# Kernel tuning notes

Measured on AMD Instinct MI355X. Metric: run time of the kernel, lower is better.

The kernel has to match this reference:

```python
import jax, jax.numpy as jnp
import numpy as np

N, E, G = 50000, 800000, 64
IN_CH, HID = 64, 64


def setup_inputs() -> dict:
    key = jax.random.key(0)
    ks = jax.random.split(key, 16)
    inp = {
        "x": jax.random.normal(ks[0], (N, IN_CH), dtype=jnp.float32),
        "edge_index": jax.random.randint(ks[1], (2, E), 0, N, dtype=jnp.int64),
        "edge_weight": jax.random.uniform(ks[2], (E,), dtype=jnp.float32),
        "batch": jnp.sort(jax.random.randint(ks[3], (N,), 0, G, dtype=jnp.int64)),
        "W1": jax.random.normal(ks[4], (IN_CH, HID), dtype=jnp.float32) / np.sqrt(IN_CH),
        "b1": jnp.zeros((HID,), dtype=jnp.float32),
        "W2": jax.random.normal(ks[5], (HID, HID), dtype=jnp.float32) / np.sqrt(HID),
        "b2": jnp.zeros((HID,), dtype=jnp.float32),
        "W3": jax.random.normal(ks[6], (HID, HID), dtype=jnp.float32) / np.sqrt(HID),
        "b3": jnp.zeros((HID,), dtype=jnp.float32),
        "lw1": jax.random.normal(ks[7], (HID, HID // 2), dtype=jnp.float32) / np.sqrt(HID),
        "lb1": jnp.zeros((HID // 2,), dtype=jnp.float32),
        "lw2": jax.random.normal(ks[8], (HID // 2, HID // 4), dtype=jnp.float32) / np.sqrt(HID // 2),
        "lb2": jnp.zeros((HID // 4,), dtype=jnp.float32),
        "lw3": jax.random.normal(ks[9], (HID // 4, 1), dtype=jnp.float32) / np.sqrt(HID // 4),
        "lb3": jnp.zeros((1,), dtype=jnp.float32),
    }
    return inp


def _gcn_layer(x, W, b, src, dst, ew):
    # GCNConv with normalize=False: transform, gather at src, weight, scatter-add at dst, + bias
    h = x @ W                                  # [N, HID]
    msg = h[src] * ew[:, None]                 # [E, HID] gather + edge weighting
    agg = jax.ops.segment_sum(msg, dst, num_segments=N)  # [N, HID] scatter-add
    return agg + b


def reference(x, edge_index, edge_weight, batch,
              W1, b1, W2, b2, W3, b3,
              lw1, lb1, lw2, lb2, lw3, lb3):
    src, dst = edge_index[0], edge_index[1]
    h = jax.nn.relu(_gcn_layer(x, W1, b1, src, dst, edge_weight))
    h = jax.nn.relu(_gcn_layer(h, W2, b2, src, dst, edge_weight))
    h = jax.nn.relu(_gcn_layer(h, W3, b3, src, dst, edge_weight))
    # global mean pool over graphs
    sums = jax.ops.segment_sum(h, batch, num_segments=G)          # [G, HID]
    cnts = jax.ops.segment_sum(jnp.ones((N,), h.dtype), batch, num_segments=G)
    pooled = sums / jnp.clip(cnts, 1.0)[:, None]
    # MLP head (dropout is identity in eval mode)
    z = jax.nn.relu(pooled @ lw1 + lb1)
    z = jax.nn.relu(z @ lw2 + lb2)
    return z @ lw3 + lb3                       # [G, 1]
```

## Files before the change

kernel.cpp:

```cpp
#include <hip/hip_runtime.h>
#include <hip/hip_bf16.h>
#include <hip/hip_fp16.h>


#define HID 64
#define KNBLK 256

__global__ __launch_bounds__(256) void histA_conv_kernel(const int* __restrict__ ei,
                                                         int* __restrict__ counts,
                                                         const float* __restrict__ x,
                                                         __half* __restrict__ xh,
                                                         int E, int K, int chunk, int n4) {
    __shared__ int hist[256];
    int t = threadIdx.x, b = blockIdx.x;
    hist[t] = 0;
    __syncthreads();
    int s = b * chunk, e1 = min(E, s + chunk);
    for (int i = s + t; i < e1; i += 256)
        atomicAdd(&hist[ei[E + i] >> 8], 1);
    for (int i = b * 256 + t; i < n4; i += 256 * KNBLK) {
        const float4 v = *reinterpret_cast<const float4*>(x + (size_t)i * 4);
        __half2 a = __float22half2_rn(make_float2(v.x, v.y));
        __half2 b2 = __float22half2_rn(make_float2(v.z, v.w));
        uint2 u;
        u.x = __builtin_bit_cast(unsigned int, a);
        u.y = __builtin_bit_cast(unsigned int, b2);
        *reinterpret_cast<uint2*>(xh + (size_t)i * 4) = u;
    }
    __syncthreads();
    if (t < K) counts[b * K + t] = hist[t];
}

__global__ __launch_bounds__(256) void scanB1_kernel(int* __restrict__ counts,
                                                     int* __restrict__ btot, int K) {
    __shared__ int sh[256];
    int k = blockIdx.x, t = threadIdx.x;
    int v = counts[t * K + k];
    sh[t] = v;
    __syncthreads();
    #pragma unroll
    for (int d = 1; d < 256; d <<= 1) {
        int add = (t >= d) ? sh[t - d] : 0;
        __syncthreads();
        sh[t] += add;
        __syncthreads();
    }
    counts[t * K + k] = sh[t] - v;
    if (t == 255) btot[k] = sh[255];
}

__global__ __launch_bounds__(256) void scanB2_kernel(const int* __restrict__ btot,
                                                     int* __restrict__ bb0, int K,
                                                     float* __restrict__ sums,
                                                     float* __restrict__ cnts, int G) {
    __shared__ int sh[256];
    int t = threadIdx.x;
    int v = (t < K) ? btot[t] : 0;
    sh[t] = v;
    __syncthreads();
    #pragma unroll
    for (int d = 1; d < 256; d <<= 1) {
        int add = (t >= d) ? sh[t - d] : 0;
        __syncthreads();
        sh[t] += add;
        __syncthreads();
    }
    if (t < K) bb0[t] = sh[t] - v;
    if (t == 255) bb0[K] = sh[255];
    for (int i = t; i < G * 64; i += 256) sums[i] = 0.f;
    if (t < G) cnts[t] = 0.f;
}

__global__ __launch_bounds__(256) void passB_kernel(const int* __restrict__ ei,
                                                    const float* __restrict__ ew,
                                                    const int* __restrict__ counts,
                                                    const int* __restrict__ bb0,
                                                    int2* __restrict__ ebuf,
                                                    int E, int K, int chunk) {
    __shared__ int lcur[256];
    int t = threadIdx.x, b = blockIdx.x;
    lcur[t] = 0;
    __syncthreads();
    int s = b * chunk, e1 = min(E, s + chunk);
    for (int i = s + t; i < e1; i += 256) {
        int src = ei[i];
        int dst = ei[E + i];
        float w = ew[i];
        int k = dst >> 8;
        int idx = atomicAdd(&lcur[k], 1);
        int slot = bb0[k] + counts[b * K + k] + idx;
        ebuf[slot] = make_int2(src | ((dst & 255) << 16), __float_as_int(w));
    }
}

__global__ __launch_bounds__(256) void passC_kernel(const int2* __restrict__ ebuf,
                                                    const int* __restrict__ bb0,
                                                    int2* __restrict__ csr,
                                                    int* __restrict__ offs,
                                                    int N, int E, int K) {
    __shared__ int ldeg[256];
    __shared__ int sh[256];
    __shared__ int lofs[256];
    int b = blockIdx.x, t = threadIdx.x;
    int gb0 = bb0[b], gb1 = bb0[b + 1];
    int cnt = gb1 - gb0;
    int base = b << 8;
    ldeg[t] = 0;
    __syncthreads();
    for (int i = t; i < cnt; i += 256)
        atomicAdd(&ldeg[(ebuf[gb0 + i].x >> 16) & 255], 1);
    __syncthreads();
    int v = ldeg[t];
    sh[t] = v;
    __syncthreads();
    #pragma unroll
    for (int d = 1; d < 256; d <<= 1) {
        int add = (t >= d) ? sh[t - d] : 0;
        __syncthreads();
        sh[t] += add;
        __syncthreads();
    }
    lofs[t] = sh[t] - v;
    int nInB = min(256, N - base);
    if (t < nInB) offs[base + t] = gb0 + lofs[t];
    if (b == K - 1 && t == 0) offs[N] = E;
    __syncthreads();
    for (int i = t; i < cnt; i += 256) {
        int2 r = ebuf[gb0 + i];
        int d = (r.x >> 16) & 255;
        int pos = atomicAdd(&lofs[d], 1);
        csr[gb0 + pos] = make_int2(r.x & 0xFFFF, r.y);
    }
}

__global__ __launch_bounds__(256) void agg_fused_kernel(const __half* __restrict__ prev,
                                                        const int2* __restrict__ csr,
                                                        const int* __restrict__ offs,
                                                        const float* __restrict__ W,
                                                        const float* __restrict__ bias,
                                                        __half* __restrict__ out, int N) {
    __shared__ float Wl[64 * 64];
    __shared__ float bl[64];
    for (int i = threadIdx.x; i < 64 * 64; i += 256) Wl[i] = W[i];
    if (threadIdx.x < 64) bl[threadIdx.x] = bias[threadIdx.x];
    __syncthreads();

    int g = (blockIdx.x * 256 + threadIdx.x) >> 3;
    int l = threadIdx.x & 7;
    if (g >= N) return;

    int e0 = offs[g], e1 = offs[g + 1];
    float acc[8] = {0.f, 0.f, 0.f, 0.f, 0.f, 0.f, 0.f, 0.f};

    #define GLOAD(R, U)                                                              \
        const uint4 U = *reinterpret_cast<const uint4*>(prev + (size_t)(R).x * 64 + l * 8);
    #define GACC(U, WW)                                                              \
        {                                                                            \
            const float2 f0 = __half22float2(__builtin_bit_cast(__half2, (U).x));    \
            const float2 f1 = __half22float2(__builtin_bit_cast(__half2, (U).y));    \
            const float2 f2 = __half22float2(__builtin_bit_cast(__half2, (U).z));    \
            const float2 f3 = __half22float2(__builtin_bit_cast(__half2, (U).w));    \
            acc[0] = fmaf((WW), f0.x, acc[0]); acc[1] = fmaf((WW), f0.y, acc[1]);    \
            acc[2] = fmaf((WW), f1.x, acc[2]); acc[3] = fmaf((WW), f1.y, acc[3]);    \
            acc[4] = fmaf((WW), f2.x, acc[4]); acc[5] = fmaf((WW), f2.y, acc[5]);    \
            acc[6] = fmaf((WW), f3.x, acc[6]); acc[7] = fmaf((WW), f3.y, acc[7]);    \
        }

    int e = e0;
    for (; e + 4 <= e1; e += 4) {
        int2 r0 = csr[e + 0];
        int2 r1 = csr[e + 1];
        int2 r2 = csr[e + 2];
        int2 r3 = csr[e + 3];
        GLOAD(r0, ua);
        GLOAD(r1, ub);
        GLOAD(r2, uc);
        GLOAD(r3, ud);
        GACC(ua, __int_as_float(r0.y));
        GACC(ub, __int_as_float(r1.y));
        GACC(uc, __int_as_float(r2.y));
        GACC(ud, __int_as_float(r3.y));
    }
    for (; e < e1; ++e) {
        int2 r = csr[e];
        GLOAD(r, ue);
        GACC(ue, __int_as_float(r.y));
    }
    #undef GLOAD
    #undef GACC

    float o[8];
    #pragma unroll
    for (int j = 0; j < 8; ++j) o[j] = bl[l * 8 + j];
    #pragma unroll
    for (int k2 = 0; k2 < 8; ++k2) {
        float c[8];
        #pragma unroll
        for (int j = 0; j < 8; ++j) c[j] = __shfl(acc[j], k2, 8);
        #pragma unroll
        for (int j = 0; j < 8; ++j) {
            const float4 wa = *reinterpret_cast<const float4*>(Wl + (8 * k2 + j) * 64 + l * 8);
            const float4 wb = *reinterpret_cast<const float4*>(Wl + (8 * k2 + j) * 64 + l * 8 + 4);
            o[0] = fmaf(c[j], wa.x, o[0]); o[1] = fmaf(c[j], wa.y, o[1]);
            o[2] = fmaf(c[j], wa.z, o[2]); o[3] = fmaf(c[j], wa.w, o[3]);
            o[4] = fmaf(c[j], wb.x, o[4]); o[5] = fmaf(c[j], wb.y, o[5]);
            o[6] = fmaf(c[j], wb.z, o[6]); o[7] = fmaf(c[j], wb.w, o[7]);
        }
    }
    uint4 u;
    u.x = __builtin_bit_cast(unsigned int,
          __float22half2_rn(make_float2(fmaxf(o[0], 0.f), fmaxf(o[1], 0.f))));
    u.y = __builtin_bit_cast(unsigned int,
          __float22half2_rn(make_float2(fmaxf(o[2], 0.f), fmaxf(o[3], 0.f))));
    u.z = __builtin_bit_cast(unsigned int,
          __float22half2_rn(make_float2(fmaxf(o[4], 0.f), fmaxf(o[5], 0.f))));
    u.w = __builtin_bit_cast(unsigned int,
          __float22half2_rn(make_float2(fmaxf(o[6], 0.f), fmaxf(o[7], 0.f))));
    *reinterpret_cast<uint4*>(out + (size_t)g * 64 + l * 8) = u;
}

__global__ __launch_bounds__(256) void pool_kernel(const __half* __restrict__ a,
                                                   const int* __restrict__ batch,
                                                   float* __restrict__ sums,
                                                   float* __restrict__ cnts, int N) {
    int c = threadIdx.x & 63;
    int sub = threadIdx.x >> 6;
    int chunk = (N + gridDim.x - 1) / gridDim.x;
    int start = blockIdx.x * chunk;
    int end = min(N, start + chunk);
    int curg = -1;
    float acc = 0.f, cacc = 0.f;
    for (int n = start + sub; n < end; n += 4) {
        int g = batch[n];
        if (g != curg) {
            if (curg >= 0) {
                atomicAdd(&sums[curg * 64 + c], acc);
                if (c == 0) atomicAdd(&cnts[curg], cacc);
            }
            curg = g; acc = 0.f; cacc = 0.f;
        }
        acc += __half2float(a[(size_t)n * 64 + c]);
        cacc += 1.f;
    }
    if (curg >= 0) {
        atomicAdd(&sums[curg * 64 + c], acc);
        if (c == 0) atomicAdd(&cnts[curg], cacc);
    }
}

__global__ __launch_bounds__(256) void head_kernel(const float* __restrict__ sums,
                                                   const float* __restrict__ cnts,
                                                   const float* __restrict__ lw1,
                                                   const float* __restrict__ lb1,
                                                   const float* __restrict__ lw2,
                                                   const float* __restrict__ lb2,
                                                   const float* __restrict__ lw3,
                                                   const float* __restrict__ lb3,
                                                   float* __restrict__ out, int G) {
    __shared__ float pooled[64 * 64];
    __shared__ float z1[64 * 32];
    __shared__ float z2[64 * 16];
    int tid = threadIdx.x;
    for (int i = tid; i < G * 64; i += 256) {
        int g = i >> 6;
        float cn = cnts[g];
        cn = (cn < 1.f) ? 1.f : cn;
        pooled[i] = sums[i] / cn;
    }
    __syncthreads();
    for (int i = tid; i < G * 32; i += 256) {
        int g = i >> 5, j = i & 31;
        float acc = lb1[j];
        #pragma unroll
        for (int k = 0; k < 64; ++k) acc = fmaf(pooled[g * 64 + k], lw1[k * 32 + j], acc);
        z1[i] = fmaxf(acc, 0.f);
    }
    __syncthreads();
    for (int i = tid; i < G * 16; i += 256) {
        int g = i >> 4, j = i & 15;
        float acc = lb2[j];
        #pragma unroll
        for (int k = 0; k < 32; ++k) acc = fmaf(z1[g * 32 + k], lw2[k * 16 + j], acc);
        z2[i] = fmaxf(acc, 0.f);
    }
    __syncthreads();
    if (tid < G) {
        float acc = lb3[0];
        #pragma unroll
        for (int k = 0; k < 16; ++k) acc = fmaf(z2[tid * 16 + k], lw3[k], acc);
        out[tid] = acc;
    }
}

static inline size_t align256(size_t x) { return (x + 255) & ~(size_t)255; }

extern "C" void kernel_launch(void* const* d_in, const int* in_sizes, int n_in,
                              void* d_out, int out_size, void* d_ws, size_t ws_size,
                              hipStream_t stream) {
    const float* x     = (const float*)d_in[0];
    const int*   ei    = (const int*)d_in[1];
    const float* ew    = (const float*)d_in[2];
    const int*   batch = (const int*)d_in[3];
    const float* W1 = (const float*)d_in[4];
    const float* b1 = (const float*)d_in[5];
    const float* W2 = (const float*)d_in[6];
    const float* b2 = (const float*)d_in[7];
    const float* W3 = (const float*)d_in[8];
    const float* b3 = (const float*)d_in[9];
    const float* lw1 = (const float*)d_in[10];
    const float* lb1 = (const float*)d_in[11];
    const float* lw2 = (const float*)d_in[12];
    const float* lb2 = (const float*)d_in[13];
    const float* lw3 = (const float*)d_in[14];
    const float* lb3 = (const float*)d_in[15];
    float* out = (float*)d_out;

    const int N = in_sizes[0] / 64;
    const int E = in_sizes[2];
    const int G = out_size;
    const int K = (N + 255) >> 8;
    const int chunk = (E + KNBLK - 1) / KNBLK;

    char* w = (char*)d_ws;
    size_t off = 0;
    auto carve = [&](size_t bytes) -> void* {
        void* p = w + off;
        off = align256(off + bytes);
        return p;
    };
    __half* xh    = (__half*)carve((size_t)N * 64 * 2);
    __half* hA    = (__half*)carve((size_t)N * 64 * 2);
    __half* hB    = (__half*)carve((size_t)N * 64 * 2);
    int2*  csr    = (int2*)carve((size_t)E * 8);
    int2*  ebuf   = (int2*)carve((size_t)E * 8);
    int*   counts = (int*)carve((size_t)KNBLK * K * 4);
    int*   btot   = (int*)carve((size_t)K * 4);
    int*   bb0    = (int*)carve((size_t)(K + 1) * 4);
    int*   offs   = (int*)carve((size_t)(N + 1) * 4);
    float* sums   = (float*)carve((size_t)G * 64 * 4);
    float* cnts   = (float*)carve((size_t)G * 4);
    (void)ws_size; (void)n_in;

    const int n4 = N * 64 / 4;

    histA_conv_kernel<<<KNBLK, 256, 0, stream>>>(ei, counts, x, xh, E, K, chunk, n4);
    scanB1_kernel<<<K,     256, 0, stream>>>(counts, btot, K);
    scanB2_kernel<<<1,     256, 0, stream>>>(btot, bb0, K, sums, cnts, G);
    passB_kernel <<<KNBLK, 256, 0, stream>>>(ei, ew, counts, bb0, ebuf, E, K, chunk);
    passC_kernel <<<K,     256, 0, stream>>>(ebuf, bb0, csr, offs, N, E, K);

    const int AGG_BLOCKS = (int)(((size_t)N * 8 + 255) / 256);

    agg_fused_kernel<<<AGG_BLOCKS, 256, 0, stream>>>(xh, csr, offs, W1, b1, hA, N);
    agg_fused_kernel<<<AGG_BLOCKS, 256, 0, stream>>>(hA, csr, offs, W2, b2, hB, N);
    agg_fused_kernel<<<AGG_BLOCKS, 256, 0, stream>>>(hB, csr, offs, W3, b3, hA, N);

    pool_kernel<<<1024, 256, 0, stream>>>(hA, batch, sums, cnts, N);
    head_kernel<<<1, 256, 0, stream>>>(sums, cnts, lw1, lb1, lw2, lb2, lw3, lb3, out, G);
}
```

Measured before the change: 157.8 us.

## Drop second scan kernel via atomic block offsets and vectorize pool loads

Removes the single-block scanB2 launch. Each scanB1 block now atomically adds its bucket total into every later entry of bb0, which histA zeroes together with sums and cnts. The pool kernel switches to 8 lanes per node, each loading 16-byte half vectors with 8 accumulators, and runs on half as many blocks. Costs are K*K/2 global atomics and a possible race, since bb0 is zeroed by block 0 of histA with no ordering against other blocks, though the kernel boundary before scanB1 makes that safe.

```diff
diff --git a/kernel.cpp b/kernel.cpp
--- a/kernel.cpp
+++ b/kernel.cpp
@@ -10,11 +10,20 @@
                                                          int* __restrict__ counts,
                                                          const float* __restrict__ x,
                                                          __half* __restrict__ xh,
-                                                         int E, int K, int chunk, int n4) {
+                                                         int* __restrict__ bb0,
+                                                         float* __restrict__ sums,
+                                                         float* __restrict__ cnts,
+                                                         int E, int K, int chunk,
+                                                         int n4, int G) {
     __shared__ int hist[256];
     int t = threadIdx.x, b = blockIdx.x;
     hist[t] = 0;
     __syncthreads();
+    if (b == 0) {
+        for (int i = t; i <= K; i += 256) bb0[i] = 0;
+        for (int i = t; i < G * 64; i += 256) sums[i] = 0.f;
+        if (t < G) cnts[t] = 0.f;
+    }
     int s = b * chunk, e1 = min(E, s + chunk);
     for (int i = s + t; i < e1; i += 256)
         atomicAdd(&hist[ei[E + i] >> 8], 1);
@@ -32,7 +41,7 @@
 }
 
 __global__ __launch_bounds__(256) void scanB1_kernel(int* __restrict__ counts,
-                                                     int* __restrict__ btot, int K) {
+                                                     int* __restrict__ bb0, int K) {
     __shared__ int sh[256];
     int k = blockIdx.x, t = threadIdx.x;
     int v = counts[t * K + k];
@@ -46,29 +55,9 @@
         __syncthreads();
     }
     counts[t * K + k] = sh[t] - v;
-    if (t == 255) btot[k] = sh[255];
-}
-
-__global__ __launch_bounds__(256) void scanB2_kernel(const int* __restrict__ btot,
-                                                     int* __restrict__ bb0, int K,
-                                                     float* __restrict__ sums,
-                                                     float* __restrict__ cnts, int G) {
-    __shared__ int sh[256];
-    int t = threadIdx.x;
-    int v = (t < K) ? btot[t] : 0;
-    sh[t] = v;
-    __syncthreads();
-    #pragma unroll
-    for (int d = 1; d < 256; d <<= 1) {
-        int add = (t >= d) ? sh[t - d] : 0;
-        __syncthreads();
-        sh[t] += add;
-        __syncthreads();
-    }
-    if (t < K) bb0[t] = sh[t] - v;
-    if (t == 255) bb0[K] = sh[255];
-    for (int i = t; i < G * 64; i += 256) sums[i] = 0.f;
-    if (t < G) cnts[t] = 0.f;
+    int total = sh[255];
+    int j = k + 1 + t;
+    if (j <= K) atomicAdd(&bb0[j], total);
 }
 
 __global__ __launch_bounds__(256) void passB_kernel(const int* __restrict__ ei,
@@ -223,28 +212,44 @@
                                                    const int* __restrict__ batch,
                                                    float* __restrict__ sums,
                                                    float* __restrict__ cnts, int N) {
-    int c = threadIdx.x & 63;
-    int sub = threadIdx.x >> 6;
+    int l = threadIdx.x & 7;
+    int sub = threadIdx.x >> 3;
     int chunk = (N + gridDim.x - 1) / gridDim.x;
     int start = blockIdx.x * chunk;
     int end = min(N, start + chunk);
     int curg = -1;
-    float acc = 0.f, cacc = 0.f;
-    for (int n = start + sub; n < end; n += 4) {
+    float acc[8] = {0.f, 0.f, 0.f, 0.f, 0.f, 0.f, 0.f, 0.f};
+    float cacc = 0.f;
+    for (int n = start + sub; n < end; n += 32) {
         int g = batch[n];
         if (g != curg) {
             if (curg >= 0) {
-                atomicAdd(&sums[curg * 64 + c], acc);
-                if (c == 0) atomicAdd(&cnts[curg], cacc);
+                #pragma unroll
+                for (int j = 0; j < 8; ++j)
+                    atomicAdd(&sums[curg * 64 + l * 8 + j], acc[j]);
+                if (l == 0) atomicAdd(&cnts[curg], cacc);
             }
-            curg = g; acc = 0.f; cacc = 0.f;
+            curg = g;
+            #pragma unroll
+            for (int j = 0; j < 8; ++j) acc[j] = 0.f;
+            cacc = 0.f;
         }
-        acc += __half2float(a[(size_t)n * 64 + c]);
+        const uint4 u = *reinterpret_cast<const uint4*>(a + (size_t)n * 64 + l * 8);
+        const float2 f0 = __half22float2(__builtin_bit_cast(__half2, u.x));
+        const float2 f1 = __half22float2(__builtin_bit_cast(__half2, u.y));
+        const float2 f2 = __half22float2(__builtin_bit_cast(__half2, u.z));
+        const float2 f3 = __half22float2(__builtin_bit_cast(__half2, u.w));
+        acc[0] += f0.x; acc[1] += f0.y;
+        acc[2] += f1.x; acc[3] += f1.y;
+        acc[4] += f2.x; acc[5] += f2.y;
+        acc[6] += f3.x; acc[7] += f3.y;
         cacc += 1.f;
     }
     if (curg >= 0) {
-        atomicAdd(&sums[curg * 64 + c], acc);
-        if (c == 0) atomicAdd(&cnts[curg], cacc);
+        #pragma unroll
+        for (int j = 0; j < 8; ++j)
+            atomicAdd(&sums[curg * 64 + l * 8 + j], acc[j]);
+        if (l == 0) atomicAdd(&cnts[curg], cacc);
     }
 }
 
@@ -334,7 +339,6 @@
     int2*  csr    = (int2*)carve((size_t)E * 8);
     int2*  ebuf   = (int2*)carve((size_t)E * 8);
     int*   counts = (int*)carve((size_t)KNBLK * K * 4);
-    int*   btot   = (int*)carve((size_t)K * 4);
     int*   bb0    = (int*)carve((size_t)(K + 1) * 4);
     int*   offs   = (int*)carve((size_t)(N + 1) * 4);
     float* sums   = (float*)carve((size_t)G * 64 * 4);
@@ -343,9 +347,9 @@
 
     const int n4 = N * 64 / 4;
 
-    histA_conv_kernel<<<KNBLK, 256, 0, stream>>>(ei, counts, x, xh, E, K, chunk, n4);
-    scanB1_kernel<<<K,     256, 0, stream>>>(counts, btot, K);
-    scanB2_kernel<<<1,     256, 0, stream>>>(btot, bb0, K, sums, cnts, G);
+    histA_conv_kernel<<<KNBLK, 256, 0, stream>>>(ei, counts, x, xh, bb0, sums, cnts,
+                                                 E, K, chunk, n4, G);
+    scanB1_kernel<<<K,     256, 0, stream>>>(counts, bb0, K);
     passB_kernel <<<KNBLK, 256, 0, stream>>>(ei, ew, counts, bb0, ebuf, E, K, chunk);
     passC_kernel <<<K,     256, 0, stream>>>(ebuf, bb0, csr, offs, N, E, K);
 
@@ -355,6 +359,6 @@
     agg_fused_kernel<<<AGG_BLOCKS, 256, 0, stream>>>(hA, csr, offs, W2, b2, hB, N);
     agg_fused_kernel<<<AGG_BLOCKS, 256, 0, stream>>>(hB, csr, offs, W3, b3, hA, N);
 
-    pool_kernel<<<1024, 256, 0, stream>>>(hA, batch, sums, cnts, N);
+    pool_kernel<<<512, 256, 0, stream>>>(hA, batch, sums, cnts, N);
     head_kernel<<<1, 256, 0, stream>>>(sums, cnts, lw1, lb1, lw2, lb2, lw3, lb3, out, G);
 }
```

Result: slower. 255.9 us (+62.1%).
